# Optimization experiments

Measured on AMD Instinct MI355X. Metric: run time of the kernel, lower is better.

Reference implementation:

```python
import jax, jax.numpy as jnp
import numpy as np


def setup_inputs() -> dict:
    key0 = jax.random.key(0)
    kq, kk, kv = jax.random.split(key0, 3)
    B, S, D = 8, 2048, 64
    return {
        "query": jax.random.normal(kq, (B, S, D), dtype=jnp.float32),
        "key": jax.random.normal(kk, (B, S, D), dtype=jnp.float32),
        "value": jax.random.normal(kv, (B, S, D), dtype=jnp.float32),
    }


def reference(query, key, value):
    # Pairwise L2 distances without materializing the [B,S,S,D] diff tensor:
    # ||q - k||^2 = ||q||^2 + ||k||^2 - 2 q.k
    q2 = jnp.sum(query * query, axis=-1)                      # [B,S]
    k2 = jnp.sum(key * key, axis=-1)                          # [B,S]
    qk = jnp.einsum("bsd,btd->bst", query, key)               # [B,S,S]
    d2 = jnp.maximum(q2[:, :, None] + k2[:, None, :] - 2.0 * qk, 0.0)
    dist = jnp.sqrt(d2)                                        # [B,S,S]
    weights = jnp.exp(-dist)
    attn = jax.nn.softmax(weights, axis=-1)                    # softmax over exp(-dist)
    # dropout is identity at inference
    return jnp.einsum("bst,btd->bsd", attn, value)
```

## Files before the change

kernel.cpp:

```cpp
#include <hip/hip_runtime.h>
#include <hip/hip_bf16.h>

#define BATCH 8
#define SEQ   2048
#define DIM   64

typedef __attribute__((ext_vector_type(8))) short short8;
typedef __attribute__((ext_vector_type(4))) float floatx4;

static __device__ __forceinline__ unsigned short f2bf(float x) {
    union { float f; unsigned u; } v; v.f = x;
    return (unsigned short)((v.u + 0x8000u) >> 16);
}

#if __has_builtin(__builtin_amdgcn_sqrtf)
#define FSQRT(x) __builtin_amdgcn_sqrtf(x)
#else
#define FSQRT(x) sqrtf(x)
#endif
#if __has_builtin(__builtin_amdgcn_exp2f)
#define FEXP2(x) __builtin_amdgcn_exp2f(x)
#else
#define FEXP2(x) exp2f(x)
#endif

static __device__ __forceinline__ void load_lds16(const void* g, void* l) {
    __builtin_amdgcn_global_load_lds(
        (const __attribute__((address_space(1))) void*)g,
        (__attribute__((address_space(3))) void*)l, 16, 0, 0);
}

#define QK_BLK 512
#define VT_BLK 256

__global__ __launch_bounds__(256) void prep_all(
        const float* __restrict__ Q, const float* __restrict__ K,
        const float* __restrict__ V,
        unsigned short* __restrict__ Qb, unsigned short* __restrict__ Kb,
        unsigned short* __restrict__ Vt,
        float* __restrict__ q2, float* __restrict__ k2,
        float* __restrict__ csum) {
    int bid = blockIdx.x;
    if (bid < QK_BLK) {
        const int NQ = BATCH * SEQ * (DIM / 4);
        #pragma unroll
        for (int ch = 0; ch < 4; ++ch) {
            int gid = ch * (QK_BLK * 256) + bid * 256 + threadIdx.x;
            const float* src; unsigned short* db; float* dn; int idx; float scl; int swz;
            if (gid < NQ) { src = Q; db = Qb; dn = q2; idx = gid;      scl = -2.f; swz = 0; }
            else          { src = K; db = Kb; dn = k2; idx = gid - NQ; scl =  1.f; swz = 1; }
            float4 v = ((const float4*)src)[idx];
            float s = v.x * v.x + v.y * v.y + v.z * v.z + v.w * v.w;
            ushort4 o;
            o.x = f2bf(v.x * scl); o.y = f2bf(v.y * scl);
            o.z = f2bf(v.z * scl); o.w = f2bf(v.w * scl);
            int row = idx >> 4, j = idx & 15;
            int jo  = swz ? (j ^ ((row & 7) << 1)) : j;
            ((ushort4*)db)[(row << 4) | jo] = o;
            s += __shfl_xor(s, 1); s += __shfl_xor(s, 2);
            s += __shfl_xor(s, 4); s += __shfl_xor(s, 8);
            if (j == 0) dn[row] = s;
        }
    } else {
        __shared__ float tile[64][65];
        __shared__ float psum[4][64];
        int vb = bid - QK_BLK;
        int b  = vb >> 5;
        int t0 = (vb & 31) * 64;
        int i  = threadIdx.x;
        int d  = i & 63, g = i >> 6;
        float part = 0.f;
        #pragma unroll
        for (int p = 0; p < 16; ++p) {
            int tt = p * 4 + g;
            float v = V[((size_t)(b * SEQ + t0 + tt)) * DIM + d];
            tile[tt][d] = v;
            part += v;
        }
        psum[g][d] = part;
        __syncthreads();
        int tt = i & 63;
        #pragma unroll
        for (int p = 0; p < 16; ++p) {
            int dd = p * 4 + g;
            Vt[((size_t)(b * DIM + dd)) * SEQ + t0 + (tt ^ ((dd & 7) << 3))] =
                f2bf(tile[tt][dd]);
        }
        if (i < 64)
            atomicAdd(&csum[b * DIM + i],
                      psum[0][i] + psum[1][i] + psum[2][i] + psum[3][i]);
    }
}

__global__ __launch_bounds__(256, 4) void gauss_attn(
        const unsigned short* __restrict__ Qb, const unsigned short* __restrict__ Kb,
        const unsigned short* __restrict__ Vt, const float* __restrict__ q2,
        const float* __restrict__ k2, float* __restrict__ denbuf,
        float* __restrict__ out) {
    __shared__ __align__(16) struct {
        unsigned short Kt[2][64 * 64];
        unsigned short Vv[2][64 * 64];
        unsigned short P[4][16 * 64];
    } sh;

    const int bid   = blockIdx.x;
    const int ts    = bid & 3;
    const int qt    = (bid >> 2) & 31;
    const int b     = bid >> 7;
    const int qb0   = qt * 64;
    const int tid   = threadIdx.x;
    const int w     = tid >> 6;
    const int lane  = tid & 63;
    const int l15   = lane & 15;
    const int quad  = lane >> 4;
    const int qrow0 = qb0 + w * 16;
    const int s7    = l15 & 7;
    const int t00   = ts * 512;

    const size_t kbase = (size_t)b * SEQ * DIM;
    const size_t vbase = (size_t)b * DIM * SEQ;

    short8 qf0 = *(const short8*)(Qb + ((size_t)(b * SEQ + qrow0 + l15)) * DIM + quad * 8);
    short8 qf1 = *(const short8*)(Qb + ((size_t)(b * SEQ + qrow0 + l15)) * DIM + 32 + quad * 8);
    floatx4 q2v = *(const floatx4*)(q2 + b * SEQ + qrow0 + quad * 4);
    const float* k2p = k2 + b * SEQ + l15;

    floatx4 acc[4];
    #pragma unroll
    for (int nt = 0; nt < 4; ++nt) acc[nt] = (floatx4){0.f, 0.f, 0.f, 0.f};
    float dsum[4] = {0.f, 0.f, 0.f, 0.f};

    unsigned short* Pw = sh.P[w];
    const float NLOG2E = -1.4426950408889634f;

    auto dma_tile = [&](int t0, int bf) {
        #pragma unroll
        for (int i = 0; i < 2; ++i) {
            int r = w * 16 + i * 8;
            load_lds16(Kb + kbase + (size_t)(t0 + r + (lane >> 3)) * DIM + (lane & 7) * 8,
                       &sh.Kt[bf][r * 64]);
            load_lds16(Vt + vbase + (size_t)(r + (lane >> 3)) * SEQ + t0 + (lane & 7) * 8,
                       &sh.Vv[bf][r * 64]);
        }
    };

    dma_tile(t00, 0);
    __syncthreads();

    #pragma unroll 1
    for (int it = 0; it < 8; ++it) {
        const int bf = it & 1;
        if (it != 7) dma_tile(t00 + (it + 1) * 64, bf ^ 1);
        const int t0 = t00 + it * 64;
        float k2n0 = k2p[t0], k2n1 = k2p[t0 + 16], k2n2 = k2p[t0 + 32], k2n3 = k2p[t0 + 48];

        const unsigned short* Kt = sh.Kt[bf];
        const unsigned short* Vv = sh.Vv[bf];

        #pragma unroll
        for (int nt = 0; nt < 4; ++nt) {
            short8 kf0 = *(const short8*)&Kt[(nt * 16 + l15) * 64 + ((quad ^ s7) << 3)];
            short8 kf1 = *(const short8*)&Kt[(nt * 16 + l15) * 64 + (((4 | quad) ^ s7) << 3)];
            float k2n = (nt == 0) ? k2n0 : (nt == 1) ? k2n1 : (nt == 2) ? k2n2 : k2n3;
            floatx4 sc;
            #pragma unroll
            for (int r = 0; r < 4; ++r) sc[r] = q2v[r] + k2n;
            sc = __builtin_amdgcn_mfma_f32_16x16x32_bf16(qf0, kf0, sc, 0, 0, 0);
            sc = __builtin_amdgcn_mfma_f32_16x16x32_bf16(qf1, kf1, sc, 0, 0, 0);
            #pragma unroll
            for (int r = 0; r < 4; ++r) {
                float d2  = fmaxf(sc[r], 0.f);
                float wgt = FEXP2(FSQRT(d2) * NLOG2E);
                float pv = wgt * fmaf(wgt, fmaf(wgt, 0.16666667f, 0.5f), 1.f);
                dsum[r] += pv;
                int row = quad * 4 + r;
                Pw[row * 64 + ((((nt << 1) | (l15 >> 3)) ^ (row & 7)) << 3) + (l15 & 7)]
                    = f2bf(pv);
            }
        }

        #pragma unroll
        for (int tc = 0; tc < 2; ++tc) {
            short8 pf = *(const short8*)&Pw[l15 * 64 + (((tc * 4 + quad) ^ s7) << 3)];
            #pragma unroll
            for (int nt = 0; nt < 4; ++nt) {
                short8 vf = *(const short8*)
                    &Vv[(nt * 16 + l15) * 64 + ((((tc << 2) | quad) ^ s7) << 3)];
                acc[nt] = __builtin_amdgcn_mfma_f32_16x16x32_bf16(pf, vf, acc[nt], 0, 0, 0);
            }
        }
        __syncthreads();
    }

    #pragma unroll
    for (int r = 0; r < 4; ++r) {
        dsum[r] += __shfl_xor(dsum[r], 1);
        dsum[r] += __shfl_xor(dsum[r], 2);
        dsum[r] += __shfl_xor(dsum[r], 4);
        dsum[r] += __shfl_xor(dsum[r], 8);
    }
    #pragma unroll
    for (int nt = 0; nt < 4; ++nt) {
        #pragma unroll
        for (int r = 0; r < 4; ++r) {
            atomicAdd(&out[((size_t)(b * SEQ + qrow0 + quad * 4 + r)) * DIM + nt * 16 + l15],
                      acc[nt][r]);
        }
    }
    if (l15 == 0) {
        #pragma unroll
        for (int r = 0; r < 4; ++r)
            atomicAdd(&denbuf[b * SEQ + qrow0 + quad * 4 + r], dsum[r]);
    }
}

__global__ __launch_bounds__(256) void finalize(
        const float* __restrict__ denbuf, const float* __restrict__ csum,
        float* __restrict__ out) {
    int gid = blockIdx.x * 256 + threadIdx.x;
    int row = gid >> 4;
    int dq  = gid & 15;
    int b   = row >> 11;
    float rcp = 1.f / (2048.f + denbuf[row]);
    float4 n = *(const float4*)(out + (size_t)row * DIM + dq * 4);
    float4 c = *(const float4*)(csum + b * DIM + dq * 4);
    float4 o = {(n.x + c.x) * rcp, (n.y + c.y) * rcp,
                (n.z + c.z) * rcp, (n.w + c.w) * rcp};
    *(float4*)(out + (size_t)row * DIM + dq * 4) = o;
}

extern "C" void kernel_launch(void* const* d_in, const int* in_sizes, int n_in,
                              void* d_out, int out_size, void* d_ws, size_t ws_size,
                              hipStream_t stream) {
    const float* Q = (const float*)d_in[0];
    const float* K = (const float*)d_in[1];
    const float* V = (const float*)d_in[2];
    float* out = (float*)d_out;

    char* ws = (char*)d_ws;
    unsigned short* Qb = (unsigned short*)(ws);
    unsigned short* Kb = (unsigned short*)(ws + (2u << 20));
    unsigned short* Vt = (unsigned short*)(ws + (4u << 20));
    float* q2     = (float*)(ws + (6u << 20));
    float* k2     = (float*)(ws + (6u << 20) + (64u << 10));
    float* csum   = (float*)(ws + (6u << 20) + (128u << 10));
    float* denbuf = (float*)(ws + (6u << 20) + (192u << 10));

    hipMemsetAsync(csum, 0, BATCH * DIM * sizeof(float), stream);
    hipMemsetAsync(denbuf, 0, BATCH * SEQ * sizeof(float), stream);
    hipMemsetAsync(out, 0, (size_t)BATCH * SEQ * DIM * sizeof(float), stream);
    prep_all<<<QK_BLK + VT_BLK, 256, 0, stream>>>(
        Q, K, V, Qb, Kb, Vt, q2, k2, csum);
    gauss_attn<<<BATCH * 32 * 4, 256, 0, stream>>>(
        Qb, Kb, Vt, q2, k2, denbuf, out);
    finalize<<<(BATCH * SEQ * DIM / 4) / 256, 256, 0, stream>>>(
        denbuf, csum, out);
}
```

Baseline: 105.2 us.

## Split key range eightfold, replace atomics with partial buffers and single-buffer LDS

Doubles the key-dimension split so 2048 blocks each process 256 keys. Each block writes its numerator and denominator partials to per-split buffers, and a reduction in finalize replaces the atomic adds and the three memsets. LDS drops from double to single buffering, with two barriers per tile, and launch bounds rise to allow 6 blocks per CU. The extra partial buffers add roughly 32MB of write and read traffic in finalize, and tile loads no longer overlap compute within a block.

```diff
diff --git a/kernel.cpp b/kernel.cpp
--- a/kernel.cpp
+++ b/kernel.cpp
@@ -4,6 +4,7 @@
 #define BATCH 8
 #define SEQ   2048
 #define DIM   64
+#define TSPLIT 8
 
 typedef __attribute__((ext_vector_type(8))) short short8;
 typedef __attribute__((ext_vector_type(4))) float floatx4;
@@ -39,7 +40,7 @@
         unsigned short* __restrict__ Qb, unsigned short* __restrict__ Kb,
         unsigned short* __restrict__ Vt,
         float* __restrict__ q2, float* __restrict__ k2,
-        float* __restrict__ csum) {
+        float* __restrict__ csum_part) {
     int bid = blockIdx.x;
     if (bid < QK_BLK) {
         const int NQ = BATCH * SEQ * (DIM / 4);
@@ -87,35 +88,34 @@
                 f2bf(tile[tt][dd]);
         }
         if (i < 64)
-            atomicAdd(&csum[b * DIM + i],
-                      psum[0][i] + psum[1][i] + psum[2][i] + psum[3][i]);
-    }
-}
-
-__global__ __launch_bounds__(256, 4) void gauss_attn(
+            csum_part[vb * 64 + i] =
+                psum[0][i] + psum[1][i] + psum[2][i] + psum[3][i];
+    }
+}
+
+__global__ __launch_bounds__(256, 6) void gauss_attn(
         const unsigned short* __restrict__ Qb, const unsigned short* __restrict__ Kb,
         const unsigned short* __restrict__ Vt, const float* __restrict__ q2,
-        const float* __restrict__ k2, float* __restrict__ denbuf,
-        float* __restrict__ out) {
+        const float* __restrict__ k2,
+        float* __restrict__ nbuf, float* __restrict__ dbuf) {
     __shared__ __align__(16) struct {
-        unsigned short Kt[2][64 * 64];
-        unsigned short Vv[2][64 * 64];
+        unsigned short Kt[64 * 64];
+        unsigned short Vv[64 * 64];
         unsigned short P[4][16 * 64];
     } sh;
 
     const int bid   = blockIdx.x;
-    const int ts    = bid & 3;
-    const int qt    = (bid >> 2) & 31;
-    const int b     = bid >> 7;
-    const int qb0   = qt * 64;
+    const int ts    = bid & 7;
+    const int qt    = (bid >> 3) & 31;
+    const int b     = bid >> 8;
     const int tid   = threadIdx.x;
     const int w     = tid >> 6;
     const int lane  = tid & 63;
     const int l15   = lane & 15;
     const int quad  = lane >> 4;
-    const int qrow0 = qb0 + w * 16;
+    const int qrow0 = qt * 64 + w * 16;
     const int s7    = l15 & 7;
-    const int t00   = ts * 512;
+    const int t00   = ts * 256;
 
     const size_t kbase = (size_t)b * SEQ * DIM;
     const size_t vbase = (size_t)b * DIM * SEQ;
@@ -133,34 +133,30 @@
     unsigned short* Pw = sh.P[w];
     const float NLOG2E = -1.4426950408889634f;
 
-    auto dma_tile = [&](int t0, int bf) {
+    auto dma_tile = [&](int t0) {
         #pragma unroll
         for (int i = 0; i < 2; ++i) {
             int r = w * 16 + i * 8;
             load_lds16(Kb + kbase + (size_t)(t0 + r + (lane >> 3)) * DIM + (lane & 7) * 8,
-                       &sh.Kt[bf][r * 64]);
+                       &sh.Kt[r * 64]);
             load_lds16(Vt + vbase + (size_t)(r + (lane >> 3)) * SEQ + t0 + (lane & 7) * 8,
-                       &sh.Vv[bf][r * 64]);
+                       &sh.Vv[r * 64]);
         }
     };
 
-    dma_tile(t00, 0);
-    __syncthreads();
-
     #pragma unroll 1
-    for (int it = 0; it < 8; ++it) {
-        const int bf = it & 1;
-        if (it != 7) dma_tile(t00 + (it + 1) * 64, bf ^ 1);
+    for (int it = 0; it < 4; ++it) {
         const int t0 = t00 + it * 64;
+        __syncthreads();
+        dma_tile(t0);
+        __syncthreads();
+
         float k2n0 = k2p[t0], k2n1 = k2p[t0 + 16], k2n2 = k2p[t0 + 32], k2n3 = k2p[t0 + 48];
 
-        const unsigned short* Kt = sh.Kt[bf];
-        const unsigned short* Vv = sh.Vv[bf];
-
         #pragma unroll
         for (int nt = 0; nt < 4; ++nt) {
-            short8 kf0 = *(const short8*)&Kt[(nt * 16 + l15) * 64 + ((quad ^ s7) << 3)];
-            short8 kf1 = *(const short8*)&Kt[(nt * 16 + l15) * 64 + (((4 | quad) ^ s7) << 3)];
+            short8 kf0 = *(const short8*)&sh.Kt[(nt * 16 + l15) * 64 + ((quad ^ s7) << 3)];
+            short8 kf1 = *(const short8*)&sh.Kt[(nt * 16 + l15) * 64 + (((4 | quad) ^ s7) << 3)];
             float k2n = (nt == 0) ? k2n0 : (nt == 1) ? k2n1 : (nt == 2) ? k2n2 : k2n3;
             floatx4 sc;
             #pragma unroll
@@ -185,11 +181,10 @@
             #pragma unroll
             for (int nt = 0; nt < 4; ++nt) {
                 short8 vf = *(const short8*)
-                    &Vv[(nt * 16 + l15) * 64 + ((((tc << 2) | quad) ^ s7) << 3)];
+                    &sh.Vv[(nt * 16 + l15) * 64 + ((((tc << 2) | quad) ^ s7) << 3)];
                 acc[nt] = __builtin_amdgcn_mfma_f32_16x16x32_bf16(pf, vf, acc[nt], 0, 0, 0);
             }
         }
-        __syncthreads();
     }
 
     #pragma unroll
@@ -199,33 +194,46 @@
         dsum[r] += __shfl_xor(dsum[r], 4);
         dsum[r] += __shfl_xor(dsum[r], 8);
     }
+    float* nb = nbuf + (size_t)ts * (BATCH * SEQ * DIM);
     #pragma unroll
     for (int nt = 0; nt < 4; ++nt) {
         #pragma unroll
         for (int r = 0; r < 4; ++r) {
-            atomicAdd(&out[((size_t)(b * SEQ + qrow0 + quad * 4 + r)) * DIM + nt * 16 + l15],
-                      acc[nt][r]);
+            nb[((size_t)(b * SEQ + qrow0 + quad * 4 + r)) * DIM + nt * 16 + l15] =
+                acc[nt][r];
         }
     }
     if (l15 == 0) {
         #pragma unroll
         for (int r = 0; r < 4; ++r)
-            atomicAdd(&denbuf[b * SEQ + qrow0 + quad * 4 + r], dsum[r]);
+            dbuf[ts * (BATCH * SEQ) + b * SEQ + qrow0 + quad * 4 + r] = dsum[r];
     }
 }
 
 __global__ __launch_bounds__(256) void finalize(
-        const float* __restrict__ denbuf, const float* __restrict__ csum,
-        float* __restrict__ out) {
+        const float* __restrict__ nbuf, const float* __restrict__ dbuf,
+        const float* __restrict__ csum_part, float* __restrict__ out) {
     int gid = blockIdx.x * 256 + threadIdx.x;
     int row = gid >> 4;
     int dq  = gid & 15;
     int b   = row >> 11;
-    float rcp = 1.f / (2048.f + denbuf[row]);
-    float4 n = *(const float4*)(out + (size_t)row * DIM + dq * 4);
-    float4 c = *(const float4*)(csum + b * DIM + dq * 4);
-    float4 o = {(n.x + c.x) * rcp, (n.y + c.y) * rcp,
-                (n.z + c.z) * rcp, (n.w + c.w) * rcp};
+    float den = 2048.f;
+    #pragma unroll
+    for (int t = 0; t < TSPLIT; ++t) den += dbuf[t * (BATCH * SEQ) + row];
+    float rcp = 1.f / den;
+    float4 n = {0.f, 0.f, 0.f, 0.f};
+    #pragma unroll
+    for (int t = 0; t < TSPLIT; ++t) {
+        float4 p = *(const float4*)(nbuf + (size_t)t * (BATCH * SEQ * DIM)
+                                         + (size_t)row * DIM + dq * 4);
+        n.x += p.x; n.y += p.y; n.z += p.z; n.w += p.w;
+    }
+    #pragma unroll 8
+    for (int t = 0; t < 32; ++t) {
+        float4 c = *(const float4*)(csum_part + (b * 32 + t) * 64 + dq * 4);
+        n.x += c.x; n.y += c.y; n.z += c.z; n.w += c.w;
+    }
+    float4 o = {n.x * rcp, n.y * rcp, n.z * rcp, n.w * rcp};
     *(float4*)(out + (size_t)row * DIM + dq * 4) = o;
 }
 
@@ -243,16 +251,14 @@
     unsigned short* Vt = (unsigned short*)(ws + (4u << 20));
     float* q2     = (float*)(ws + (6u << 20));
     float* k2     = (float*)(ws + (6u << 20) + (64u << 10));
-    float* csum   = (float*)(ws + (6u << 20) + (128u << 10));
-    float* denbuf = (float*)(ws + (6u << 20) + (192u << 10));
-
-    hipMemsetAsync(csum, 0, BATCH * DIM * sizeof(float), stream);
-    hipMemsetAsync(denbuf, 0, BATCH * SEQ * sizeof(float), stream);
-    hipMemsetAsync(out, 0, (size_t)BATCH * SEQ * DIM * sizeof(float), stream);
+    float* cpart  = (float*)(ws + (6u << 20) + (128u << 10));
+    float* dbuf   = (float*)(ws + (6u << 20) + (192u << 10));
+    float* nbuf   = (float*)(ws + (7u << 20));
+
     prep_all<<<QK_BLK + VT_BLK, 256, 0, stream>>>(
-        Q, K, V, Qb, Kb, Vt, q2, k2, csum);
-    gauss_attn<<<BATCH * 32 * 4, 256, 0, stream>>>(
-        Qb, Kb, Vt, q2, k2, denbuf, out);
+        Q, K, V, Qb, Kb, Vt, q2, k2, cpart);
+    gauss_attn<<<BATCH * 32 * TSPLIT, 256, 0, stream>>>(
+        Qb, Kb, Vt, q2, k2, nbuf, dbuf);
     finalize<<<(BATCH * SEQ * DIM / 4) / 256, 256, 0, stream>>>(
-        denbuf, csum, out);
-}
+        nbuf, dbuf, cpart, out);
+}
```

Measured after the change: 105.3 us. No clear change (+0.2%).
